# Kernel optimization log

Measured on AMD Instinct MI355X. Metric: run time of the kernel, lower is better.

The kernel has to match this reference:

```python
import jax, jax.numpy as jnp
import numpy as np

IMAGE_SIZE = 800
OUT = 50          # feature map size
FEAT = 512
SCALES = (2.0, 4.0, 6.0)
RATIOS = (0.5, 1.0, 1.5)
A = len(SCALES) * len(RATIOS)          # 9 anchors per cell
POS_THR, NEG_THR = 0.7, 0.3
W_CONF, W_REG = 1.0, 5.0
SCALE = IMAGE_SIZE // OUT              # 16, stride of feature map


def _anchor_base():
    # order: ratio outer loop, scale inner loop (matches get_anchor_base)
    ws = jnp.array([s * r for r in RATIOS for s in SCALES], jnp.float32)  # [A]
    hs = jnp.array([s for r in RATIOS for s in SCALES], jnp.float32)      # [A]
    cx = (jnp.arange(OUT, dtype=jnp.float32) + 0.5)[:, None, None]        # grid dim0 -> x
    cy = (jnp.arange(OUT, dtype=jnp.float32) + 0.5)[None, :, None]        # grid dim1 -> y
    xmin = jnp.clip(cx - ws / 2, 0.0, OUT)
    xmax = jnp.clip(cx + ws / 2, 0.0, OUT)
    ymin = jnp.clip(cy - hs / 2, 0.0, OUT)
    ymax = jnp.clip(cy + hs / 2, 0.0, OUT)
    shp = (OUT, OUT, A)
    base = jnp.stack([jnp.broadcast_to(xmin, shp), jnp.broadcast_to(ymin, shp),
                      jnp.broadcast_to(xmax, shp), jnp.broadcast_to(ymax, shp)], axis=-1)
    return base.reshape(-1, 4)         # [N,4], N = OUT*OUT*A = 22500


def _iou(anchors, gt):
    # anchors [N,4], gt [B,M,4] (xyxy) -> iou [B,N,M]
    a = anchors[None, :, None, :]
    g = gt[:, None, :, :]
    ix1 = jnp.maximum(a[..., 0], g[..., 0]); iy1 = jnp.maximum(a[..., 1], g[..., 1])
    ix2 = jnp.minimum(a[..., 2], g[..., 2]); iy2 = jnp.minimum(a[..., 3], g[..., 3])
    inter = jnp.clip(ix2 - ix1, 0.0) * jnp.clip(iy2 - iy1, 0.0)
    area_a = (a[..., 2] - a[..., 0]) * (a[..., 3] - a[..., 1])
    area_g = (g[..., 2] - g[..., 0]) * (g[..., 3] - g[..., 1])
    return inter / (area_a + area_g - inter + 1e-8)


def _smooth_l1(d):
    ad = jnp.abs(d)
    return jnp.where(ad < 1.0, 0.5 * d * d, ad - 0.5)


def setup_inputs() -> dict:
    key = jax.random.key(0)
    ks = jax.random.split(key, 8)
    B, M = 16, 16
    features = jax.random.normal(ks[0], (B, FEAT, OUT, OUT), jnp.float32)
    # valid GT boxes in image coords: centers in [100,700], sizes in [32,200]
    cxy = jax.random.uniform(ks[1], (B, M, 2), jnp.float32, 100.0, 700.0)
    wh = jax.random.uniform(ks[2], (B, M, 2), jnp.float32, 32.0, 200.0)
    x1y1 = jnp.clip(cxy - wh / 2, 0.0, IMAGE_SIZE)
    x2y2 = jnp.clip(cxy + wh / 2, 0.0, IMAGE_SIZE)
    gt_boxes = jnp.concatenate([x1y1, x2y2], axis=-1)
    w1 = jax.random.normal(ks[3], (FEAT, FEAT, 3, 3), jnp.float32) * 0.02
    b1 = jnp.zeros((FEAT,), jnp.float32)
    w_cls = jax.random.normal(ks[4], (A, FEAT), jnp.float32) * 0.02
    b_cls = jnp.zeros((A,), jnp.float32)
    w_box = jax.random.normal(ks[5], (4 * A, FEAT), jnp.float32) * 0.02
    b_box = jnp.zeros((4 * A,), jnp.float32)
    return {"features": features, "gt_boxes": gt_boxes, "w1": w1, "b1": b1,
            "w_cls": w_cls, "b_cls": b_cls, "w_box": w_box, "b_box": b_box}


def reference(features, gt_boxes, w1, b1, w_cls, b_cls, w_box, b_box):
    B = features.shape[0]
    anchors = _anchor_base()                                   # [N,4]
    N = anchors.shape[0]

    # --- conv tower ---
    x = jax.lax.conv_general_dilated(features, w1, (1, 1), 'SAME') + b1[None, :, None, None]
    cls_map = jnp.einsum('bchw,ac->bahw', x, w_cls) + b_cls[None, :, None, None]   # [B,A,H,W]
    box_map = jnp.einsum('bchw,dc->bdhw', x, w_box) + b_box[None, :, None, None]   # [B,4A,H,W]
    logits = jnp.transpose(cls_map, (0, 2, 3, 1)).reshape(B, N)                    # [B,N]
    pred_off = jnp.transpose(box_map.reshape(B, A, 4, OUT, OUT), (0, 3, 4, 1, 2)).reshape(B, N, 4)

    # --- project gt to feature-map (anchor) coords, 'p2a' ---
    gt = gt_boxes / SCALE                                       # [B,M,4]

    # --- anchor/GT assignment ---
    iou = _iou(anchors, gt)                                     # [B,N,M]
    max_per_gt = jnp.max(iou, axis=1, keepdims=True)            # best anchor per gt
    pos_mask = ((iou == max_per_gt) & (max_per_gt > 0)) | (iou > POS_THR)  # [B,N,M]
    pos_mask = pos_mask.astype(jnp.float32)
    n_pos = jnp.maximum(pos_mask.sum(), 1.0)

    # --- gt offsets (standard tx,ty,tw,th) for every (anchor,gt) pair ---
    acx = (anchors[:, 0] + anchors[:, 2]) / 2
    acy = (anchors[:, 1] + anchors[:, 3]) / 2
    aw = jnp.maximum(anchors[:, 2] - anchors[:, 0], 1e-6)
    ah = jnp.maximum(anchors[:, 3] - anchors[:, 1], 1e-6)
    gcx = (gt[..., 0] + gt[..., 2]) / 2                         # [B,M]
    gcy = (gt[..., 1] + gt[..., 3]) / 2
    gw = jnp.maximum(gt[..., 2] - gt[..., 0], 1e-6)
    gh = jnp.maximum(gt[..., 3] - gt[..., 1], 1e-6)
    tx = (gcx[:, None, :] - acx[None, :, None]) / aw[None, :, None]   # [B,N,M]
    ty = (gcy[:, None, :] - acy[None, :, None]) / ah[None, :, None]
    tw = jnp.log(gw[:, None, :] / aw[None, :, None])
    th = jnp.log(gh[:, None, :] / ah[None, :, None])
    gt_off = jnp.stack([tx, ty, tw, th], axis=-1)               # [B,N,M,4]

    diff = gt_off - pred_off[:, :, None, :]
    reg_loss = (pos_mask[..., None] * _smooth_l1(diff)).sum() / (4.0 * n_pos)

    # --- classification loss: BCE-with-logits; positives=1, negatives=0 ---
    pos_loss = (pos_mask * jax.nn.softplus(-logits)[:, :, None]).sum() / n_pos
    neg_anchor = jnp.all(iou < NEG_THR, axis=2).astype(jnp.float32)   # [B,N]
    n_neg = jnp.maximum(neg_anchor.sum(), 1.0)
    neg_loss = (neg_anchor * jax.nn.softplus(logits)).sum() / n_neg
    cls_loss = 0.5 * (pos_loss + neg_loss)

    total_rpn_loss = W_CONF * cls_loss + W_REG * reg_loss

    # --- proposals from predicted offsets for all anchors ---
    pcx = acx[None, :] + pred_off[..., 0] * aw[None, :]
    pcy = acy[None, :] + pred_off[..., 1] * ah[None, :]
    pw = aw[None, :] * jnp.exp(pred_off[..., 2])
    ph = ah[None, :] * jnp.exp(pred_off[..., 3])
    proposals = jnp.stack([pcx - pw / 2, pcy - ph / 2, pcx + pw / 2, pcy + ph / 2], axis=-1)  # [B,N,4]

    return total_rpn_loss, proposals
```

## Files before the change

kernel.cpp:

```cpp
#include <hip/hip_runtime.h>
#include <hip/hip_bf16.h>
#include <stdint.h>


using bf16x8 = __attribute__((ext_vector_type(8))) __bf16;
using f32x4  = __attribute__((ext_vector_type(4))) float;

#define FT_CHUNK_STRIDE 2768896
#define W2_CHUNK_B 27648

__device__ __forceinline__ unsigned short f2bf(float f) {
  union { float f; unsigned u; } x; x.f = f;
  unsigned r = x.u + 0x7fffu + ((x.u >> 16) & 1u);
  return (unsigned short)(r >> 16);
}

__device__ __forceinline__ void gl_lds16(const void* g, void* l) {
  __builtin_amdgcn_global_load_lds(
      (const __attribute__((address_space(1))) void*)g,
      (__attribute__((address_space(3))) void*)l, 16, 0, 0);
}

__device__ __forceinline__ float sl1(float d) {
  float ad = fabsf(d);
  return ad < 1.f ? 0.5f * d * d : ad - 0.5f;
}
__device__ __forceinline__ float softplus_f(float x) {
  return fmaxf(x, 0.f) + log1pf(expf(-fabsf(x)));
}

__device__ __forceinline__ void anchor_strict(int n, float& ax1, float& ay1,
                                              float& ax2, float& ay2) {
  int ii = n / 450;
  int rem = n - ii * 450;
  int jj = rem / 9;
  int a  = rem - jj * 9;
  const float SC[3] = {2.f, 4.f, 6.f};
  const float RA[3] = {0.5f, 1.f, 1.5f};
  float w = __fmul_rn(SC[a % 3], RA[a / 3]);
  float h = SC[a % 3];
  float cx = __fadd_rn((float)ii, 0.5f);
  float cy = __fadd_rn((float)jj, 0.5f);
  float wh = __fmul_rn(w, 0.5f), hh = __fmul_rn(h, 0.5f);
  ax1 = fminf(fmaxf(__fsub_rn(cx, wh), 0.f), 50.f);
  ax2 = fminf(fmaxf(__fadd_rn(cx, wh), 0.f), 50.f);
  ay1 = fminf(fmaxf(__fsub_rn(cy, hh), 0.f), 50.f);
  ay2 = fminf(fmaxf(__fadd_rn(cy, hh), 0.f), 50.f);
}
__device__ __forceinline__ float iou_strict(float ax1, float ay1, float ax2, float ay2,
                                            float aarea, const float* __restrict__ g) {
  float gx1 = __fmul_rn(g[0], 0.0625f), gy1 = __fmul_rn(g[1], 0.0625f);
  float gx2 = __fmul_rn(g[2], 0.0625f), gy2 = __fmul_rn(g[3], 0.0625f);
  float ix1 = fmaxf(ax1, gx1), iy1 = fmaxf(ay1, gy1);
  float ix2 = fminf(ax2, gx2), iy2 = fminf(ay2, gy2);
  float inter = __fmul_rn(fmaxf(__fsub_rn(ix2, ix1), 0.f),
                          fmaxf(__fsub_rn(iy2, iy1), 0.f));
  float garea = __fmul_rn(__fsub_rn(gx2, gx1), __fsub_rn(gy2, gy1));
  float denom = __fadd_rn(__fsub_rn(__fadd_rn(aarea, garea), inter), 1e-8f);
  return __fdiv_rn(inter, denom);
}

__global__ __launch_bounds__(256, 4) void k1(const float* __restrict__ feat,
                                             char* __restrict__ featT2,
                                             const float* __restrict__ w1,
                                             const float* __restrict__ wc,
                                             const float* __restrict__ wb,
                                             const float* __restrict__ b1,
                                             const float* __restrict__ bc,
                                             const float* __restrict__ bbx,
                                             float* __restrict__ part,
                                             float* __restrict__ bias_eff,
                                             unsigned* __restrict__ zbuf) {
  __shared__ __align__(16) char smem[128 * 132 * 2];
  const int bxr = blockIdx.x;
  const int tid = threadIdx.x;

  if (bxr < 576) {
    if (bxr == 0) {
      if (tid < 256) zbuf[tid] = 0u;
      if (tid < 8) zbuf[256 + tid] = 0u;
    }
    int cz = bxr / 72, kx = bxr - cz * 72;
    float* sW = (float*)smem;
#pragma unroll
    for (int q = 0; q < 12; ++q) {
      int idx = tid + q * 256;
      int co = idx >> 6, cl = idx & 63;
      int c = cz * 64 + cl;
      float v = 0.f;
      if (co < 9) v = wc[co * 512 + c];
      else if (co < 45) v = wb[(co - 9) * 512 + c];
      sW[co * 64 + cl] = v;
    }
    __syncthreads();
    const int kmem = kx * 64 + (tid & 63);
    const int coq  = tid >> 6;
    float acc[12];
#pragma unroll
    for (int j = 0; j < 12; ++j) acc[j] = 0.f;
    const float* w1p = w1 + (size_t)(cz * 64) * 4608 + kmem;
    for (int c4 = 0; c4 < 64; c4 += 4) {
      float f0 = w1p[(size_t)(c4 + 0) * 4608];
      float f1 = w1p[(size_t)(c4 + 1) * 4608];
      float f2 = w1p[(size_t)(c4 + 2) * 4608];
      float f3 = w1p[(size_t)(c4 + 3) * 4608];
#pragma unroll
      for (int j = 0; j < 12; ++j) {
        float4 wv = *(const float4*)&sW[(coq * 12 + j) * 64 + c4];
        acc[j] += wv.x * f0 + wv.y * f1 + wv.z * f2 + wv.w * f3;
      }
    }
    float* dst = part + (size_t)cz * 221184 + kmem;
#pragma unroll
    for (int j = 0; j < 12; ++j) dst[(size_t)(coq * 12 + j) * 4608] = acc[j];
    return;
  }

  if (bxr < 624) {
    int co = bxr - 576;
    int l = tid;
    if (l >= 64) return;
    float s = 0.f;
#pragma unroll
    for (int q = 0; q < 8; ++q) {
      int c = q * 64 + l;
      float wv = co < 9 ? wc[co * 512 + c] : (co < 45 ? wb[(co - 9) * 512 + c] : 0.f);
      s += wv * b1[c];
    }
    for (int o = 32; o; o >>= 1) s += __shfl_down(s, o, 64);
    if (l == 0)
      bias_eff[co] = s + (co < 9 ? bc[co] : (co < 45 ? bbx[co - 9] : 0.f));
    return;
  }

  const int bxr2 = bxr - 624;
  const int tile = bxr2 % 21;
  const int rest = bxr2 / 21;
  const int g    = rest & 3;
  const int b    = rest >> 2;
  if (tile == 20) {
    uint4 z = {0, 0, 0, 0};
    for (int u = tid; u < 204 * 4; u += 256) {
      int p = u & 255; if (p >= 204) p -= 204;
      int c4 = u / 204;
      int ip, jp;
      if (p < 52)       { ip = 0;       jp = p; }
      else if (p < 104) { ip = 51;      jp = p - 52; }
      else if (p < 154) { ip = p - 103; jp = 0; }
      else              { ip = p - 153; jp = 51; }
      char* dst = featT2 + (size_t)(g * 4 + c4) * FT_CHUNK_STRIDE
                + (size_t)(b * 2704 + ip * 52 + jp) * 64;
      *(uint4*)(dst)      = z;
      *(uint4*)(dst + 16) = z;
      *(uint4*)(dst + 32) = z;
      *(uint4*)(dst + 48) = z;
    }
    return;
  }
  unsigned short* sT = (unsigned short*)smem;
  const int pos0 = tile * 128;
  const float* fb = feat + (size_t)b * 1280000 + (size_t)(g * 128) * 2500;
  const int pq = tid & 31;
  const int rg = tid >> 5;
  const int p  = pos0 + pq * 4;
  float vv[16][4];
  if (p + 3 < 2500) {
#pragma unroll
    for (int it = 0; it < 4; ++it)
#pragma unroll
      for (int q = 0; q < 4; ++q) {
        float4 v = *(const float4*)(fb + (size_t)(it * 32 + rg * 4 + q) * 2500 + p);
        vv[it * 4 + q][0] = v.x; vv[it * 4 + q][1] = v.y;
        vv[it * 4 + q][2] = v.z; vv[it * 4 + q][3] = v.w;
      }
  } else {
#pragma unroll
    for (int it = 0; it < 4; ++it)
#pragma unroll
      for (int q = 0; q < 4; ++q)
#pragma unroll
        for (int e = 0; e < 4; ++e)
          vv[it * 4 + q][e] = fb[(size_t)(it * 32 + rg * 4 + q) * 2500 + min(p + e, 2499)];
  }
#pragma unroll
  for (int it = 0; it < 4; ++it) {
    int cb = it * 32 + rg * 4;
#pragma unroll
    for (int pp = 0; pp < 4; ++pp) {
      ushort4 pk;
      pk.x = f2bf(vv[it * 4 + 0][pp]); pk.y = f2bf(vv[it * 4 + 1][pp]);
      pk.z = f2bf(vv[it * 4 + 2][pp]); pk.w = f2bf(vv[it * 4 + 3][pp]);
      *(ushort4*)&sT[(pq * 4 + pp) * 132 + cb] = pk;
    }
  }
  __syncthreads();
#pragma unroll
  for (int q2 = 0; q2 < 2; ++q2) {
    int u = tid + q2 * 256;
    int ch = u >> 7, pr = u & 127;
    int gp = pos0 + pr;
    if (gp >= 2500) continue;
    int i = gp / 50, j = gp - i * 50;
    char* dst = featT2 + (size_t)(g * 4 + ch) * FT_CHUNK_STRIDE
              + (size_t)(b * 2704 + (i + 1) * 52 + (j + 1)) * 64;
    const uint4* src = (const uint4*)&sT[pr * 132 + ch * 32];
    uint4 a0 = src[0], a1 = src[1], a2 = src[2], a3 = src[3];
    *(uint4*)(dst)      = a0;
    *(uint4*)(dst + 16) = a1;
    *(uint4*)(dst + 32) = a2;
    *(uint4*)(dst + 48) = a3;
  }
}

__global__ __launch_bounds__(256) void k2(const float* __restrict__ part,
                                          unsigned short* __restrict__ w2,
                                          const float* __restrict__ gt_boxes,
                                          unsigned* __restrict__ mx) {
  if (blockIdx.x >= 864) {
    int q = blockIdx.x - 864;
    int b = q / 88, nb = q - b * 88;
    int n = nb * 256 + threadIdx.x;
    float lm[16];
#pragma unroll
    for (int m = 0; m < 16; ++m) lm[m] = 0.f;
    if (n < 22500) {
      float ax1, ay1, ax2, ay2;
      anchor_strict(n, ax1, ay1, ax2, ay2);
      float aarea = __fmul_rn(__fsub_rn(ax2, ax1), __fsub_rn(ay2, ay1));
#pragma unroll
      for (int m = 0; m < 16; ++m)
        lm[m] = iou_strict(ax1, ay1, ax2, ay2, aarea, gt_boxes + (b * 16 + m) * 4);
    }
    __shared__ float red[4][16];
#pragma unroll
    for (int m = 0; m < 16; ++m) {
      float v = lm[m];
      for (int o = 32; o; o >>= 1) v = fmaxf(v, __shfl_down(v, o, 64));
      if ((threadIdx.x & 63) == 0) red[threadIdx.x >> 6][m] = v;
    }
    __syncthreads();
    if (threadIdx.x < 16) {
      float v = fmaxf(fmaxf(red[0][threadIdx.x], red[1][threadIdx.x]),
                      fmaxf(red[2][threadIdx.x], red[3][threadIdx.x]));
      atomicMax(mx + b * 16 + threadIdx.x, __float_as_uint(v));
    }
    return;
  }
  int co = blockIdx.x / 18, kx = blockIdx.x - co * 18;
  int kmem = kx * 256 + threadIdx.x;
  const float* p = part + (size_t)co * 4608 + kmem;
  float s = 0.f;
#pragma unroll
  for (int cz = 0; cz < 8; ++cz) s += p[(size_t)cz * 221184];
  int ci = kmem / 9, tap = kmem - ci * 9;
  int c = ci >> 5, e = ci & 31;
  int boff = c * W2_CHUNK_B + tap * 3072 + (co >> 4) * 1024 + (co & 15) * 64
           + ((((e >> 3) ^ co) & 3) << 4) + ((e & 7) << 1);
  w2[boff >> 1] = f2bf(s);
}

__global__ __launch_bounds__(256, 2) void k3(const char* __restrict__ featT2,
                                             const char* __restrict__ w2g,
                                             const float* __restrict__ beff,
                                             float* __restrict__ oh) {
  __shared__ __align__(16) char sF[2][11264];
  __shared__ __align__(16) char sA[2][27648];
  const int tid = threadIdx.x, lane = tid & 63, w = tid >> 6;
  const int bx0 = blockIdx.x;
  const int bx = ((bx0 & 7) << 6) | (bx0 >> 3);
  const int b = bx >> 5, tl = bx & 31, tr = tl >> 3, tc = tl & 7;
  const int i0 = tr * 13 - (tr == 3 ? 1 : 0);
  const int TI = (tr >= 2) ? 12 : 13;
  const int TJ = (tc < 2) ? 7 : 6;
  const int j0 = (tc < 2) ? tc * 7 : 14 + (tc - 2) * 6;
  const int TJ2 = TJ + 2;
  const int mcount = TI * TJ;
  const int pieces = (TI + 2) * TJ2 * 5;

  const char* srcF[3];
#pragma unroll
  for (int k = 0; k < 3; ++k) {
    int s = w * 3 + k;
    int pi = s * 64 + lane;
    if (pi >= pieces) pi = pieces - 1;
    int pos = pi / 5, pc = pi - pos * 5;
    if (pc > 3) pc = 3;
    int hi = pos / TJ2, hj = pos - hi * TJ2;
    srcF[k] = featT2 + (size_t)(b * 2704 + (i0 + hi) * 52 + (j0 + hj)) * 64 + pc * 16;
  }
  int idxB[2];
#pragma unroll
  for (int bf = 0; bf < 2; ++bf) {
    int p = (w * 2 + bf) * 16 + (lane & 15);
    if (p >= mcount) p = mcount - 1;
    int di = p / TJ, dj = p - di * TJ;
    idxB[bf] = (di * TJ2 + dj) * 80 + (lane >> 4) * 16;
  }
  const int aoff = (lane & 15) * 64 + ((((lane >> 4) ^ lane) & 3) << 4);
  int toff[9];
#pragma unroll
  for (int tp = 0; tp < 9; ++tp) toff[tp] = ((tp / 3) * TJ2 + (tp % 3)) * 80;

  f32x4 acc[3][2] = {};

  auto stage = [&](int c, int pb) {
    size_t coff = (size_t)c * FT_CHUNK_STRIDE;
#pragma unroll
    for (int k = 0; k < 3; ++k) {
      int s = w * 3 + k;
      if (s < 11) gl_lds16(srcF[k] + coff, sF[pb] + s * 1024);
    }
#pragma unroll
    for (int k = 0; k < 7; ++k) {
      int s = w + 4 * k;
      if (s < 27)
        gl_lds16(w2g + (size_t)c * W2_CHUNK_B + s * 1024 + lane * 16, sA[pb] + s * 1024);
    }
  };

  stage(0, 0);
  __builtin_amdgcn_s_waitcnt(0);
  __syncthreads();

  for (int c = 0; c < 16; ++c) {
    int pb = c & 1;
    if (c < 15) stage(c + 1, pb ^ 1);
    const char* fA = sA[pb];
    const char* fB = sF[pb];
#pragma unroll
    for (int tp = 0; tp < 9; ++tp) {
      bf16x8 av[3], bv[2];
#pragma unroll
      for (int cf = 0; cf < 3; ++cf)
        av[cf] = *(const bf16x8*)(fA + tp * 3072 + cf * 1024 + aoff);
#pragma unroll
      for (int bf = 0; bf < 2; ++bf)
        bv[bf] = *(const bf16x8*)(fB + idxB[bf] + toff[tp]);
#pragma unroll
      for (int cf = 0; cf < 3; ++cf)
#pragma unroll
        for (int bf = 0; bf < 2; ++bf)
          acc[cf][bf] = __builtin_amdgcn_mfma_f32_16x16x32_bf16(av[cf], bv[bf], acc[cf][bf], 0, 0, 0);
    }
    __builtin_amdgcn_s_waitcnt(0);
    __syncthreads();
  }

  f32x4 bias[3];
#pragma unroll
  for (int cf = 0; cf < 3; ++cf)
    bias[cf] = *(const f32x4*)(beff + cf * 16 + (lane >> 4) * 4);
#pragma unroll
  for (int bf = 0; bf < 2; ++bf) {
    int p = (w * 2 + bf) * 16 + (lane & 15);
    if (p >= mcount) continue;
    int di = p / TJ, dj = p - di * TJ;
    int gm = (b * 50 + i0 + di) * 50 + (j0 + dj);
#pragma unroll
    for (int cf = 0; cf < 3; ++cf) {
      f32x4 v = acc[cf][bf];
#pragma unroll
      for (int r = 0; r < 4; ++r) v[r] += bias[cf][r];
      *(f32x4*)(oh + (size_t)gm * 48 + cf * 16 + (lane >> 4) * 4) = v;
    }
  }
}

__global__ __launch_bounds__(256) void k4(const float* __restrict__ gt_boxes,
                                          const unsigned* __restrict__ mxbuf,
                                          const float* __restrict__ oh,
                                          float* __restrict__ accum,
                                          float* __restrict__ dout) {
  int b = blockIdx.y;
  int n = blockIdx.x * 256 + threadIdx.x;
  float s_np = 0.f, s_reg = 0.f, s_pos = 0.f, s_nc = 0.f, s_nl = 0.f;
  if (n < 22500) {
    float ax1, ay1, ax2, ay2;
    anchor_strict(n, ax1, ay1, ax2, ay2);
    float aarea = __fmul_rn(__fsub_rn(ax2, ax1), __fsub_rn(ay2, ay1));
    float acx = (ax1 + ax2) * 0.5f, acy = (ay1 + ay2) * 0.5f;
    float aw = fmaxf(ax2 - ax1, 1e-6f), ah = fmaxf(ay2 - ay1, 1e-6f);
    int ii = n / 450, rem = n - ii * 450, jj = rem / 9, a = rem - jj * 9;
    const float* row = oh + ((size_t)(b * 2500 + ii * 50 + jj)) * 48;
    float logit = row[a];
    float p0 = row[9 + a * 4], p1 = row[10 + a * 4];
    float p2 = row[11 + a * 4], p3 = row[12 + a * 4];
    int npos = 0;
    bool allneg = true;
#pragma unroll
    for (int m = 0; m < 16; ++m) {
      const float* g = gt_boxes + (b * 16 + m) * 4;
      float iou = iou_strict(ax1, ay1, ax2, ay2, aarea, g);
      float mxv = __uint_as_float(mxbuf[b * 16 + m]);
      bool pos = ((iou == mxv) && (mxv > 0.f)) || (iou > 0.7f);
      if (iou >= 0.3f) allneg = false;
      if (pos) {
        ++npos;
        float gx1 = g[0] * 0.0625f, gy1 = g[1] * 0.0625f;
        float gx2 = g[2] * 0.0625f, gy2 = g[3] * 0.0625f;
        float gcx = (gx1 + gx2) * 0.5f, gcy = (gy1 + gy2) * 0.5f;
        float gw = fmaxf(gx2 - gx1, 1e-6f), gh = fmaxf(gy2 - gy1, 1e-6f);
        float tx = (gcx - acx) / aw, ty = (gcy - acy) / ah;
        float twv = logf(gw / aw), thv = logf(gh / ah);
        s_reg += sl1(tx - p0) + sl1(ty - p1) + sl1(twv - p2) + sl1(thv - p3);
      }
    }
    s_np = (float)npos;
    s_pos = (float)npos * softplus_f(-logit);
    if (allneg) { s_nc = 1.f; s_nl = softplus_f(logit); }
    float pcx = acx + p0 * aw, pcy = acy + p1 * ah;
    float pw = aw * expf(p2), ph = ah * expf(p3);
    float* o = dout + 1 + ((size_t)b * 22500 + n) * 4;
    o[0] = pcx - pw * 0.5f;
    o[1] = pcy - ph * 0.5f;
    o[2] = pcx + pw * 0.5f;
    o[3] = pcy + ph * 0.5f;
  }
  float vals[5] = {s_np, s_reg, s_pos, s_nc, s_nl};
  __shared__ float red[4][5];
#pragma unroll
  for (int q = 0; q < 5; ++q) {
    float v = vals[q];
    for (int o = 32; o; o >>= 1) v += __shfl_down(v, o, 64);
    if ((threadIdx.x & 63) == 0) red[threadIdx.x >> 6][q] = v;
  }
  __syncthreads();
  if (threadIdx.x < 5) {
    float v = red[0][threadIdx.x] + red[1][threadIdx.x] +
              red[2][threadIdx.x] + red[3][threadIdx.x];
    atomicAdd(accum + threadIdx.x, v);
  }
  __syncthreads();
  if (threadIdx.x == 0) {
    __threadfence();
    unsigned old = atomicAdd((unsigned*)(accum + 5), 1u);
    if (old == 1407u) {
      float np = fmaxf(atomicAdd(accum + 0, 0.f), 1.f);
      float rg = atomicAdd(accum + 1, 0.f);
      float pp = atomicAdd(accum + 2, 0.f);
      float nn = fmaxf(atomicAdd(accum + 3, 0.f), 1.f);
      float nl = atomicAdd(accum + 4, 0.f);
      dout[0] = 0.5f * (pp / np + nl / nn) + 5.f * (rg / (4.f * np));
    }
  }
}

extern "C" void kernel_launch(void* const* d_in, const int* in_sizes, int n_in,
                              void* d_out, int out_size, void* d_ws, size_t ws_size,
                              hipStream_t stream) {
  const float* features = (const float*)d_in[0];
  const float* gt_boxes = (const float*)d_in[1];
  const float* w1    = (const float*)d_in[2];
  const float* b1    = (const float*)d_in[3];
  const float* w_cls = (const float*)d_in[4];
  const float* b_cls = (const float*)d_in[5];
  const float* w_box = (const float*)d_in[6];
  const float* b_box = (const float*)d_in[7];
  float* out = (float*)d_out;
  char* ws = (char*)d_ws;

  char*           featT2 = ws;
  unsigned short* w2     = (unsigned short*)(ws + 44302336);
  float*          wpart  = (float*)(ws + 44855296);
  float*          oh     = (float*)(ws + 51933184);
  float*          beff   = (float*)(ws + 59613184);
  unsigned*       mx     = (unsigned*)(ws + 59613376);
  float*          accum  = (float*)(ws + 59614400);

  k1<<<1968, 256, 0, stream>>>(features, featT2, w1, w_cls, w_box, b1, b_cls,
                               b_box, wpart, beff, mx);
  k2<<<2272, 256, 0, stream>>>(wpart, w2, gt_boxes, mx);
  k3<<<512, 256, 0, stream>>>(featT2, (const char*)w2, beff, oh);
  k4<<<dim3(88, 16), 256, 0, stream>>>(gt_boxes, mx, oh, accum, out);
}
```

Before: 251.4 us.

## Move per-GT max IoU into k1, halve transpose tiles, process two anchors per thread

The max-IoU reduction moves from k2 into k1. Each block now owns one GT box and loops over all anchors, so the atomicMax and zero-init are replaced by direct writes. The feature transpose tiles shrink from 128 to 64 positions, which doubles the block count and halves LDS use, likely to raise occupancy. In k4 each thread handles two anchors, and the GT-derived terms are precomputed once in shared memory. Together this removes redundant per-anchor GT arithmetic and rebalances the work, at the cost of a long serial 22500-anchor loop in 256 blocks inside k1.

```diff
diff --git a/kernel.cpp b/kernel.cpp
--- a/kernel.cpp
+++ b/kernel.cpp
@@ -47,17 +47,22 @@
   ay1 = fminf(fmaxf(__fsub_rn(cy, hh), 0.f), 50.f);
   ay2 = fminf(fmaxf(__fadd_rn(cy, hh), 0.f), 50.f);
 }
+__device__ __forceinline__ float iou_pre(float ax1, float ay1, float ax2, float ay2,
+                                         float aarea, const float* __restrict__ s) {
+  float ix1 = fmaxf(ax1, s[0]), iy1 = fmaxf(ay1, s[1]);
+  float ix2 = fminf(ax2, s[2]), iy2 = fminf(ay2, s[3]);
+  float inter = __fmul_rn(fmaxf(__fsub_rn(ix2, ix1), 0.f),
+                          fmaxf(__fsub_rn(iy2, iy1), 0.f));
+  float denom = __fadd_rn(__fsub_rn(__fadd_rn(aarea, s[4]), inter), 1e-8f);
+  return __fdiv_rn(inter, denom);
+}
 __device__ __forceinline__ float iou_strict(float ax1, float ay1, float ax2, float ay2,
                                             float aarea, const float* __restrict__ g) {
-  float gx1 = __fmul_rn(g[0], 0.0625f), gy1 = __fmul_rn(g[1], 0.0625f);
-  float gx2 = __fmul_rn(g[2], 0.0625f), gy2 = __fmul_rn(g[3], 0.0625f);
-  float ix1 = fmaxf(ax1, gx1), iy1 = fmaxf(ay1, gy1);
-  float ix2 = fminf(ax2, gx2), iy2 = fminf(ay2, gy2);
-  float inter = __fmul_rn(fmaxf(__fsub_rn(ix2, ix1), 0.f),
-                          fmaxf(__fsub_rn(iy2, iy1), 0.f));
-  float garea = __fmul_rn(__fsub_rn(gx2, gx1), __fsub_rn(gy2, gy1));
-  float denom = __fadd_rn(__fsub_rn(__fadd_rn(aarea, garea), inter), 1e-8f);
-  return __fdiv_rn(inter, denom);
+  float s[5];
+  s[0] = __fmul_rn(g[0], 0.0625f); s[1] = __fmul_rn(g[1], 0.0625f);
+  s[2] = __fmul_rn(g[2], 0.0625f); s[3] = __fmul_rn(g[3], 0.0625f);
+  s[4] = __fmul_rn(__fsub_rn(s[2], s[0]), __fsub_rn(s[3], s[1]));
+  return iou_pre(ax1, ay1, ax2, ay2, aarea, s);
 }
 
 __global__ __launch_bounds__(256, 4) void k1(const float* __restrict__ feat,
@@ -70,16 +75,15 @@
                                              const float* __restrict__ bbx,
                                              float* __restrict__ part,
                                              float* __restrict__ bias_eff,
-                                             unsigned* __restrict__ zbuf) {
-  __shared__ __align__(16) char smem[128 * 132 * 2];
+                                             const float* __restrict__ gt_boxes,
+                                             unsigned* __restrict__ mx,
+                                             unsigned* __restrict__ accz) {
+  __shared__ __align__(16) char smem[64 * 132 * 2];
   const int bxr = blockIdx.x;
   const int tid = threadIdx.x;
 
   if (bxr < 576) {
-    if (bxr == 0) {
-      if (tid < 256) zbuf[tid] = 0u;
-      if (tid < 8) zbuf[256 + tid] = 0u;
-    }
+    if (bxr == 0 && tid < 8) accz[tid] = 0u;
     int cz = bxr / 72, kx = bxr - cz * 72;
     float* sW = (float*)smem;
 #pragma unroll
@@ -133,12 +137,38 @@
     return;
   }
 
-  const int bxr2 = bxr - 624;
-  const int tile = bxr2 % 21;
-  const int rest = bxr2 / 21;
+  if (bxr < 880) {
+    int q = bxr - 624;
+    int b = q >> 4, m = q & 15;
+    const float* g = gt_boxes + (b * 16 + m) * 4;
+    float s[5];
+    s[0] = __fmul_rn(g[0], 0.0625f); s[1] = __fmul_rn(g[1], 0.0625f);
+    s[2] = __fmul_rn(g[2], 0.0625f); s[3] = __fmul_rn(g[3], 0.0625f);
+    s[4] = __fmul_rn(__fsub_rn(s[2], s[0]), __fsub_rn(s[3], s[1]));
+    float best = 0.f;
+    for (int n = tid; n < 22500; n += 256) {
+      float ax1, ay1, ax2, ay2;
+      anchor_strict(n, ax1, ay1, ax2, ay2);
+      float aarea = __fmul_rn(__fsub_rn(ax2, ax1), __fsub_rn(ay2, ay1));
+      best = fmaxf(best, iou_pre(ax1, ay1, ax2, ay2, aarea, s));
+    }
+    for (int o = 32; o; o >>= 1) best = fmaxf(best, __shfl_down(best, o, 64));
+    float* red = (float*)smem;
+    if ((tid & 63) == 0) red[tid >> 6] = best;
+    __syncthreads();
+    if (tid == 0) {
+      float v = fmaxf(fmaxf(red[0], red[1]), fmaxf(red[2], red[3]));
+      mx[b * 16 + m] = __float_as_uint(v);
+    }
+    return;
+  }
+
+  const int bxr2 = bxr - 880;
+  const int tile = bxr2 % 41;
+  const int rest = bxr2 / 41;
   const int g    = rest & 3;
   const int b    = rest >> 2;
-  if (tile == 20) {
+  if (tile == 40) {
     uint4 z = {0, 0, 0, 0};
     for (int u = tid; u < 204 * 4; u += 256) {
       int p = u & 255; if (p >= 204) p -= 204;
@@ -158,94 +188,60 @@
     return;
   }
   unsigned short* sT = (unsigned short*)smem;
-  const int pos0 = tile * 128;
+  const int pos0 = tile * 64;
   const float* fb = feat + (size_t)b * 1280000 + (size_t)(g * 128) * 2500;
-  const int pq = tid & 31;
-  const int rg = tid >> 5;
+  const int pq = tid & 15;
+  const int cq = tid >> 4;
   const int p  = pos0 + pq * 4;
-  float vv[16][4];
+  float vv[2][4][4];
   if (p + 3 < 2500) {
 #pragma unroll
-    for (int it = 0; it < 4; ++it)
+    for (int it = 0; it < 2; ++it)
 #pragma unroll
       for (int q = 0; q < 4; ++q) {
-        float4 v = *(const float4*)(fb + (size_t)(it * 32 + rg * 4 + q) * 2500 + p);
-        vv[it * 4 + q][0] = v.x; vv[it * 4 + q][1] = v.y;
-        vv[it * 4 + q][2] = v.z; vv[it * 4 + q][3] = v.w;
+        float4 v = *(const float4*)(fb + (size_t)(it * 64 + cq * 4 + q) * 2500 + p);
+        vv[it][q][0] = v.x; vv[it][q][1] = v.y;
+        vv[it][q][2] = v.z; vv[it][q][3] = v.w;
       }
   } else {
 #pragma unroll
-    for (int it = 0; it < 4; ++it)
+    for (int it = 0; it < 2; ++it)
 #pragma unroll
       for (int q = 0; q < 4; ++q)
 #pragma unroll
         for (int e = 0; e < 4; ++e)
-          vv[it * 4 + q][e] = fb[(size_t)(it * 32 + rg * 4 + q) * 2500 + min(p + e, 2499)];
-  }
-#pragma unroll
-  for (int it = 0; it < 4; ++it) {
-    int cb = it * 32 + rg * 4;
+          vv[it][q][e] = fb[(size_t)(it * 64 + cq * 4 + q) * 2500 + min(p + e, 2499)];
+  }
+#pragma unroll
+  for (int it = 0; it < 2; ++it) {
 #pragma unroll
     for (int pp = 0; pp < 4; ++pp) {
       ushort4 pk;
-      pk.x = f2bf(vv[it * 4 + 0][pp]); pk.y = f2bf(vv[it * 4 + 1][pp]);
-      pk.z = f2bf(vv[it * 4 + 2][pp]); pk.w = f2bf(vv[it * 4 + 3][pp]);
-      *(ushort4*)&sT[(pq * 4 + pp) * 132 + cb] = pk;
+      pk.x = f2bf(vv[it][0][pp]); pk.y = f2bf(vv[it][1][pp]);
+      pk.z = f2bf(vv[it][2][pp]); pk.w = f2bf(vv[it][3][pp]);
+      *(ushort4*)&sT[(pq * 4 + pp) * 132 + it * 64 + cq * 4] = pk;
     }
   }
   __syncthreads();
-#pragma unroll
-  for (int q2 = 0; q2 < 2; ++q2) {
-    int u = tid + q2 * 256;
-    int ch = u >> 7, pr = u & 127;
+  {
+    int ch = tid >> 6, pr = tid & 63;
     int gp = pos0 + pr;
-    if (gp >= 2500) continue;
-    int i = gp / 50, j = gp - i * 50;
-    char* dst = featT2 + (size_t)(g * 4 + ch) * FT_CHUNK_STRIDE
-              + (size_t)(b * 2704 + (i + 1) * 52 + (j + 1)) * 64;
-    const uint4* src = (const uint4*)&sT[pr * 132 + ch * 32];
-    uint4 a0 = src[0], a1 = src[1], a2 = src[2], a3 = src[3];
-    *(uint4*)(dst)      = a0;
-    *(uint4*)(dst + 16) = a1;
-    *(uint4*)(dst + 32) = a2;
-    *(uint4*)(dst + 48) = a3;
+    if (gp < 2500) {
+      int i = gp / 50, j = gp - i * 50;
+      char* dst = featT2 + (size_t)(g * 4 + ch) * FT_CHUNK_STRIDE
+                + (size_t)(b * 2704 + (i + 1) * 52 + (j + 1)) * 64;
+      const uint4* src = (const uint4*)&sT[pr * 132 + ch * 32];
+      uint4 a0 = src[0], a1 = src[1], a2 = src[2], a3 = src[3];
+      *(uint4*)(dst)      = a0;
+      *(uint4*)(dst + 16) = a1;
+      *(uint4*)(dst + 32) = a2;
+      *(uint4*)(dst + 48) = a3;
+    }
   }
 }
 
 __global__ __launch_bounds__(256) void k2(const float* __restrict__ part,
-                                          unsigned short* __restrict__ w2,
-                                          const float* __restrict__ gt_boxes,
-                                          unsigned* __restrict__ mx) {
-  if (blockIdx.x >= 864) {
-    int q = blockIdx.x - 864;
-    int b = q / 88, nb = q - b * 88;
-    int n = nb * 256 + threadIdx.x;
-    float lm[16];
-#pragma unroll
-    for (int m = 0; m < 16; ++m) lm[m] = 0.f;
-    if (n < 22500) {
-      float ax1, ay1, ax2, ay2;
-      anchor_strict(n, ax1, ay1, ax2, ay2);
-      float aarea = __fmul_rn(__fsub_rn(ax2, ax1), __fsub_rn(ay2, ay1));
-#pragma unroll
-      for (int m = 0; m < 16; ++m)
-        lm[m] = iou_strict(ax1, ay1, ax2, ay2, aarea, gt_boxes + (b * 16 + m) * 4);
-    }
-    __shared__ float red[4][16];
-#pragma unroll
-    for (int m = 0; m < 16; ++m) {
-      float v = lm[m];
-      for (int o = 32; o; o >>= 1) v = fmaxf(v, __shfl_down(v, o, 64));
-      if ((threadIdx.x & 63) == 0) red[threadIdx.x >> 6][m] = v;
-    }
-    __syncthreads();
-    if (threadIdx.x < 16) {
-      float v = fmaxf(fmaxf(red[0][threadIdx.x], red[1][threadIdx.x]),
-                      fmaxf(red[2][threadIdx.x], red[3][threadIdx.x]));
-      atomicMax(mx + b * 16 + threadIdx.x, __float_as_uint(v));
-    }
-    return;
-  }
+                                          unsigned short* __restrict__ w2) {
   int co = blockIdx.x / 18, kx = blockIdx.x - co * 18;
   int kmem = kx * 256 + threadIdx.x;
   const float* p = part + (size_t)co * 4608 + kmem;
@@ -371,70 +367,123 @@
                                           const float* __restrict__ oh,
                                           float* __restrict__ accum,
                                           float* __restrict__ dout) {
-  int b = blockIdx.y;
-  int n = blockIdx.x * 256 + threadIdx.x;
+  const int tid = threadIdx.x;
+  const int b = blockIdx.y;
+  __shared__ float sg[16][10];
+  if (tid < 16) {
+    const float* g = gt_boxes + (b * 16 + tid) * 4;
+    float gx1 = __fmul_rn(g[0], 0.0625f), gy1 = __fmul_rn(g[1], 0.0625f);
+    float gx2 = __fmul_rn(g[2], 0.0625f), gy2 = __fmul_rn(g[3], 0.0625f);
+    sg[tid][0] = gx1; sg[tid][1] = gy1; sg[tid][2] = gx2; sg[tid][3] = gy2;
+    sg[tid][4] = __fmul_rn(__fsub_rn(gx2, gx1), __fsub_rn(gy2, gy1));
+    sg[tid][5] = (gx1 + gx2) * 0.5f;
+    sg[tid][6] = (gy1 + gy2) * 0.5f;
+    sg[tid][7] = fmaxf(gx2 - gx1, 1e-6f);
+    sg[tid][8] = fmaxf(gy2 - gy1, 1e-6f);
+  }
+  __syncthreads();
+
+  const int n0 = blockIdx.x * 512 + tid;
+  const int n1 = n0 + 256;
+  const bool vA = n0 < 22500, vB = n1 < 22500;
   float s_np = 0.f, s_reg = 0.f, s_pos = 0.f, s_nc = 0.f, s_nl = 0.f;
-  if (n < 22500) {
-    float ax1, ay1, ax2, ay2;
-    anchor_strict(n, ax1, ay1, ax2, ay2);
-    float aarea = __fmul_rn(__fsub_rn(ax2, ax1), __fsub_rn(ay2, ay1));
-    float acx = (ax1 + ax2) * 0.5f, acy = (ay1 + ay2) * 0.5f;
-    float aw = fmaxf(ax2 - ax1, 1e-6f), ah = fmaxf(ay2 - ay1, 1e-6f);
-    int ii = n / 450, rem = n - ii * 450, jj = rem / 9, a = rem - jj * 9;
+
+  float Aax1 = 0, Aay1 = 0, Aax2 = 0, Aay2 = 0, Aarea = 0, Aacx = 0, Aacy = 0,
+        Aaw = 1, Aah = 1, Alog = 0, Ap0 = 0, Ap1 = 0, Ap2 = 0, Ap3 = 0;
+  float Bax1 = 0, Bay1 = 0, Bax2 = 0, Bay2 = 0, Barea = 0, Bacx = 0, Bacy = 0,
+        Baw = 1, Bah = 1, Blog = 0, Bp0 = 0, Bp1 = 0, Bp2 = 0, Bp3 = 0;
+  int npA = 0, npB = 0;
+  bool anA = true, anB = true;
+
+  if (vA) {
+    anchor_strict(n0, Aax1, Aay1, Aax2, Aay2);
+    Aarea = __fmul_rn(__fsub_rn(Aax2, Aax1), __fsub_rn(Aay2, Aay1));
+    Aacx = (Aax1 + Aax2) * 0.5f; Aacy = (Aay1 + Aay2) * 0.5f;
+    Aaw = fmaxf(Aax2 - Aax1, 1e-6f); Aah = fmaxf(Aay2 - Aay1, 1e-6f);
+    int ii = n0 / 450, rem = n0 - ii * 450, jj = rem / 9, a = rem - jj * 9;
     const float* row = oh + ((size_t)(b * 2500 + ii * 50 + jj)) * 48;
-    float logit = row[a];
-    float p0 = row[9 + a * 4], p1 = row[10 + a * 4];
-    float p2 = row[11 + a * 4], p3 = row[12 + a * 4];
-    int npos = 0;
-    bool allneg = true;
-#pragma unroll
-    for (int m = 0; m < 16; ++m) {
-      const float* g = gt_boxes + (b * 16 + m) * 4;
-      float iou = iou_strict(ax1, ay1, ax2, ay2, aarea, g);
-      float mxv = __uint_as_float(mxbuf[b * 16 + m]);
-      bool pos = ((iou == mxv) && (mxv > 0.f)) || (iou > 0.7f);
-      if (iou >= 0.3f) allneg = false;
+    Alog = row[a];
+    Ap0 = row[9 + a * 4]; Ap1 = row[10 + a * 4];
+    Ap2 = row[11 + a * 4]; Ap3 = row[12 + a * 4];
+  }
+  if (vB) {
+    anchor_strict(n1, Bax1, Bay1, Bax2, Bay2);
+    Barea = __fmul_rn(__fsub_rn(Bax2, Bax1), __fsub_rn(Bay2, Bay1));
+    Bacx = (Bax1 + Bax2) * 0.5f; Bacy = (Bay1 + Bay2) * 0.5f;
+    Baw = fmaxf(Bax2 - Bax1, 1e-6f); Bah = fmaxf(Bay2 - Bay1, 1e-6f);
+    int ii = n1 / 450, rem = n1 - ii * 450, jj = rem / 9, a = rem - jj * 9;
+    const float* row = oh + ((size_t)(b * 2500 + ii * 50 + jj)) * 48;
+    Blog = row[a];
+    Bp0 = row[9 + a * 4]; Bp1 = row[10 + a * 4];
+    Bp2 = row[11 + a * 4]; Bp3 = row[12 + a * 4];
+  }
+
+#pragma unroll
+  for (int m = 0; m < 16; ++m) {
+    const float* s = sg[m];
+    float mxv = __uint_as_float(mxbuf[b * 16 + m]);
+    float iouA = vA ? iou_pre(Aax1, Aay1, Aax2, Aay2, Aarea, s) : 0.f;
+    float iouB = vB ? iou_pre(Bax1, Bay1, Bax2, Bay2, Barea, s) : 0.f;
+    if (vA) {
+      bool pos = ((iouA == mxv) && (mxv > 0.f)) || (iouA > 0.7f);
+      if (iouA >= 0.3f) anA = false;
       if (pos) {
-        ++npos;
-        float gx1 = g[0] * 0.0625f, gy1 = g[1] * 0.0625f;
-        float gx2 = g[2] * 0.0625f, gy2 = g[3] * 0.0625f;
-        float gcx = (gx1 + gx2) * 0.5f, gcy = (gy1 + gy2) * 0.5f;
-        float gw = fmaxf(gx2 - gx1, 1e-6f), gh = fmaxf(gy2 - gy1, 1e-6f);
-        float tx = (gcx - acx) / aw, ty = (gcy - acy) / ah;
-        float twv = logf(gw / aw), thv = logf(gh / ah);
-        s_reg += sl1(tx - p0) + sl1(ty - p1) + sl1(twv - p2) + sl1(thv - p3);
+        ++npA;
+        float tx = (s[5] - Aacx) / Aaw, ty = (s[6] - Aacy) / Aah;
+        float twv = logf(s[7] / Aaw), thv = logf(s[8] / Aah);
+        s_reg += sl1(tx - Ap0) + sl1(ty - Ap1) + sl1(twv - Ap2) + sl1(thv - Ap3);
       }
     }
-    s_np = (float)npos;
-    s_pos = (float)npos * softplus_f(-logit);
-    if (allneg) { s_nc = 1.f; s_nl = softplus_f(logit); }
-    float pcx = acx + p0 * aw, pcy = acy + p1 * ah;
-    float pw = aw * expf(p2), ph = ah * expf(p3);
-    float* o = dout + 1 + ((size_t)b * 22500 + n) * 4;
-    o[0] = pcx - pw * 0.5f;
-    o[1] = pcy - ph * 0.5f;
-    o[2] = pcx + pw * 0.5f;
-    o[3] = pcy + ph * 0.5f;
-  }
+    if (vB) {
+      bool pos = ((iouB == mxv) && (mxv > 0.f)) || (iouB > 0.7f);
+      if (iouB >= 0.3f) anB = false;
+      if (pos) {
+        ++npB;
+        float tx = (s[5] - Bacx) / Baw, ty = (s[6] - Bacy) / Bah;
+        float twv = logf(s[7] / Baw), thv = logf(s[8] / Bah);
+        s_reg += sl1(tx - Bp0) + sl1(ty - Bp1) + sl1(twv - Bp2) + sl1(thv - Bp3);
+      }
+    }
+  }
+  if (vA) {
+    s_np += (float)npA;
+    s_pos += (float)npA * softplus_f(-Alog);
+    if (anA) { s_nc += 1.f; s_nl += softplus_f(Alog); }
+    float pcx = Aacx + Ap0 * Aaw, pcy = Aacy + Ap1 * Aah;
+    float pw = Aaw * expf(Ap2), ph = Aah * expf(Ap3);
+    float* o = dout + 1 + ((size_t)b * 22500 + n0) * 4;
+    o[0] = pcx - pw * 0.5f; o[1] = pcy - ph * 0.5f;
+    o[2] = pcx + pw * 0.5f; o[3] = pcy + ph * 0.5f;
+  }
+  if (vB) {
+    s_np += (float)npB;
+    s_pos += (float)npB * softplus_f(-Blog);
+    if (anB) { s_nc += 1.f; s_nl += softplus_f(Blog); }
+    float pcx = Bacx + Bp0 * Baw, pcy = Bacy + Bp1 * Bah;
+    float pw = Baw * expf(Bp2), ph = Bah * expf(Bp3);
+    float* o = dout + 1 + ((size_t)b * 22500 + n1) * 4;
+    o[0] = pcx - pw * 0.5f; o[1] = pcy - ph * 0.5f;
+    o[2] = pcx + pw * 0.5f; o[3] = pcy + ph * 0.5f;
+  }
+
   float vals[5] = {s_np, s_reg, s_pos, s_nc, s_nl};
   __shared__ float red[4][5];
 #pragma unroll
   for (int q = 0; q < 5; ++q) {
     float v = vals[q];
     for (int o = 32; o; o >>= 1) v += __shfl_down(v, o, 64);
-    if ((threadIdx.x & 63) == 0) red[threadIdx.x >> 6][q] = v;
+    if ((tid & 63) == 0) red[tid >> 6][q] = v;
   }
   __syncthreads();
-  if (threadIdx.x < 5) {
-    float v = red[0][threadIdx.x] + red[1][threadIdx.x] +
-              red[2][threadIdx.x] + red[3][threadIdx.x];
-    atomicAdd(accum + threadIdx.x, v);
+  if (tid < 5) {
+    float v = red[0][tid] + red[1][tid] + red[2][tid] + red[3][tid];
+    atomicAdd(accum + tid, v);
   }
   __syncthreads();
-  if (threadIdx.x == 0) {
+  if (tid == 0) {
     __threadfence();
     unsigned old = atomicAdd((unsigned*)(accum + 5), 1u);
-    if (old == 1407u) {
+    if (old == 703u) {
       float np = fmaxf(atomicAdd(accum + 0, 0.f), 1.f);
       float rg = atomicAdd(accum + 1, 0.f);
       float pp = atomicAdd(accum + 2, 0.f);
@@ -467,9 +516,10 @@
   unsigned*       mx     = (unsigned*)(ws + 59613376);
   float*          accum  = (float*)(ws + 59614400);
 
-  k1<<<1968, 256, 0, stream>>>(features, featT2, w1, w_cls, w_box, b1, b_cls,
-                               b_box, wpart, beff, mx);
-  k2<<<2272, 256, 0, stream>>>(wpart, w2, gt_boxes, mx);
+  k1<<<3504, 256, 0, stream>>>(features, featT2, w1, w_cls, w_box, b1, b_cls,
+                               b_box, wpart, beff, gt_boxes, mx,
+                               (unsigned*)accum);
+  k2<<<864, 256, 0, stream>>>(wpart, w2);
   k3<<<512, 256, 0, stream>>>(featT2, (const char*)w2, beff, oh);
-  k4<<<dim3(88, 16), 256, 0, stream>>>(gt_boxes, mx, oh, accum, out);
-}
+  k4<<<dim3(44, 16), 256, 0, stream>>>(gt_boxes, mx, oh, accum, out);
+}
```

Result: faster. 238.1 us (-5.3%).
